# Optimization experiments

Measured on AMD Instinct MI355X. Metric: run time of the kernel, lower is better.

## Reference

```python
import jax, jax.numpy as jnp
import numpy as np

B, T, D = 2, 2048, 2048
H, G, HD = 16, 4, 128
SCALE = 0.08838834764831845  # 1/sqrt(head_dim)
THETA = 10000.0
EPS = 1e-10


def _rope(x):
    # x: [B, T, h, HD]; faithful to source: cos/sin built from cat([freqs, freqs])
    hd = x.shape[-1]
    pos = jnp.arange(x.shape[1], dtype=x.dtype)
    inv_freq = 1.0 / (THETA ** (jnp.arange(0, hd, 2, dtype=x.dtype) / hd))
    freqs = pos[:, None] * inv_freq[None, :]            # [T, hd/2]
    emb = jnp.concatenate([freqs, freqs], axis=-1)      # [T, hd]
    cos = jnp.cos(emb)[None, :, None, :]
    sin = jnp.sin(emb)[None, :, None, :]
    x_even, x_odd = x[..., ::2], x[..., 1::2]
    rotated = jnp.stack((-x_odd, x_even), axis=-1).reshape(x.shape)
    return x * cos + rotated * sin


def _qk_norm(x):
    # F.normalize(p=2): x / clamp_min(||x||, eps)
    n = jnp.sqrt(jnp.sum(x * x, axis=-1, keepdims=True))
    return x / jnp.maximum(n, EPS)


def setup_inputs() -> dict:
    key = jax.random.key(0)
    k1, k2, k3 = jax.random.split(key, 3)
    x = jax.random.normal(k1, (B, T, D), dtype=jnp.float32)
    w_qkv = jax.random.normal(k2, (H * HD + 2 * G * HD, D), dtype=jnp.float32) * 0.02
    w_o = jax.random.normal(k3, (D, D), dtype=jnp.float32) * 0.02
    padding_mask = jnp.ones((B, T), dtype=bool)
    return {"x": x, "w_qkv": w_qkv, "w_o": w_o, "padding_mask": padding_mask,
            "use_qk_norm": 1, "use_mqa": 0}


def reference(x, w_qkv, w_o, padding_mask, use_qk_norm, use_mqa):
    qkv = jnp.einsum('btd,ed->bte', x, w_qkv)           # fused QKV projection
    q = qkv[..., :H * HD].reshape(B, T, H, HD)
    k = qkv[..., H * HD:H * HD + G * HD].reshape(B, T, G, HD)
    v = qkv[..., H * HD + G * HD:].reshape(B, T, G, HD)
    if use_qk_norm:
        q = _qk_norm(q)
        k = _qk_norm(k)
    q = _rope(q)
    k = _rope(k)
    if not use_mqa:
        rep = H // G
        k = jnp.repeat(k, rep, axis=2)                  # [B, T, H, HD]
        v = jnp.repeat(v, rep, axis=2)
    # attention: scores [B, H, Tq, Tk]
    scores = jnp.einsum('bqhd,bkhd->bhqk', q, k) * SCALE
    # faithful mask expansion: padding_mask[:, None, :, None] -> [B,1,Tq,Tk]
    mask = padding_mask[:, None, :, None]
    scores = jnp.where(mask, scores, jnp.finfo(scores.dtype).min)
    attn = jax.nn.softmax(scores, axis=-1)
    out = jnp.einsum('bhqk,bkhd->bqhd', attn, v).reshape(B, T, D)
    return jnp.einsum('btd,od->bto', out, w_o)
```

## Files before the change

### kernel.cpp

```cpp
#include <hip/hip_runtime.h>
#include <hip/hip_bf16.h>
#include <math.h>

#define B_SZ 2
#define T_SEQ 2048
#define D_MODEL 2048
#define NH 16
#define NG 4
#define HD 128
#define E_QKV 3072
#define SCALE_F 0.08838834764831845f

typedef __attribute__((ext_vector_type(8))) short short8;
typedef __attribute__((ext_vector_type(8))) _Float16 half8;
typedef __attribute__((ext_vector_type(4))) float f32x4;
typedef __attribute__((ext_vector_type(16))) float f32x16;
typedef __attribute__((ext_vector_type(4))) uint uint4v;

__device__ inline ushort f2bf(float f) {
    union { float f; uint u; } v; v.f = f;
    uint r = (v.u + 0x7FFFu + ((v.u >> 16) & 1u)) >> 16;
    return (ushort)r;
}
__device__ inline ushort f2h(float f) {
    union { _Float16 h; ushort u; } v;
    v.h = (_Float16)f;
    return v.u;
}

__device__ inline void glds16(const void* g, void* l) {
    __builtin_amdgcn_global_load_lds(
        (const __attribute__((address_space(1))) unsigned int*)g,
        (__attribute__((address_space(3))) unsigned int*)l,
        16, 0, 0);
}

__device__ inline uint cvtpk(float a, float b) {
    uint r;
    asm("v_cvt_pk_bf16_f32 %0, %1, %2" : "=v"(r) : "v"(a), "v"(b));
    return r;
}
__device__ inline void pl32swap(uint& a, uint& b) {
    asm("v_permlane32_swap_b32 %0, %1" : "+v"(a), "+v"(b));
}

__global__ __launch_bounds__(256) void cvt_f16_all(const float* __restrict__ x,
                                                   const float* __restrict__ wq,
                                                   const float* __restrict__ wo,
                                                   ushort* __restrict__ x16,
                                                   ushort* __restrict__ wq16,
                                                   ushort* __restrict__ wo16,
                                                   int n4x, int n4q, int n4o) {
    int i = blockIdx.x * 256 + threadIdx.x;
    const float* src;
    ushort* dst;
    if (i < n4x)                { src = x;  dst = x16; }
    else if (i < n4x + n4q)     { src = wq; dst = wq16; i -= n4x; }
    else if (i < n4x + n4q + n4o) { src = wo; dst = wo16; i -= n4x + n4q; }
    else return;
    float4 v = ((const float4*)src)[i];
    uint2 ho;
    ho.x = (uint)f2h(v.x) | ((uint)f2h(v.y) << 16);
    ho.y = (uint)f2h(v.z) | ((uint)f2h(v.w) << 16);
    ((uint2*)dst)[i] = ho;
}

__global__ __launch_bounds__(256) void rope_tab(float2* __restrict__ Rt) {
    int i = blockIdx.x * 256 + threadIdx.x;
    if (i >= T_SEQ * 64) return;
    int t = i >> 6, j = i & 63;
    float inv_freq = exp2f(-0.2076205059304595f * (float)j);
    float sn, cs;
    sincosf((float)t * inv_freq, &sn, &cs);
    Rt[i] = make_float2(cs, sn);
}

template <bool QKV>
__global__ __launch_bounds__(256, 3)
void gemm_f16(const ushort* __restrict__ A,
              const ushort* __restrict__ B,
              float* __restrict__ C,
              ushort* __restrict__ Qb,
              ushort* __restrict__ Kb,
              ushort* __restrict__ Vt,
              const float2* __restrict__ Rt,
              int M, int N, int K) {
    __shared__ __attribute__((aligned(16))) ushort smem[16384];
    ushort* sA = smem;
    ushort* sB = smem + 8192;

    const int tid  = threadIdx.x;
    const int wave = tid >> 6;
    const int lane = tid & 63;
    const int c    = lane & 15;
    const int quad = lane >> 4;
    const int wr   = wave >> 1;
    const int wc   = wave & 1;
    const size_t m0 = (size_t)blockIdx.y * 128;
    const size_t n0 = (size_t)blockIdx.x * 128;

    const int srow = lane >> 3;
    const int sg   = ((lane & 7) ^ (srow & 7)) * 8;
    const ushort* gsrc;
    ushort* sdst;
    if (wave < 2) {
        gsrc = A + (m0 + wave * 64 + srow) * (size_t)K + sg;
        sdst = sA + wave * 4096;
    } else {
        gsrc = B + (n0 + (wave - 2) * 64 + srow) * (size_t)K + sg;
        sdst = sB + (wave - 2) * 4096;
    }

    f32x4 acc[4][4];
#pragma unroll
    for (int i = 0; i < 4; ++i)
#pragma unroll
        for (int j = 0; j < 4; ++j) acc[i][j] = (f32x4){0.f, 0.f, 0.f, 0.f};

    const int cg = c & 7;

    for (int k0 = 0; k0 < K; k0 += 64) {
        if (k0) __syncthreads();
#pragma unroll
        for (int i = 0; i < 8; ++i)
            glds16(gsrc + (size_t)(i * 8) * K + k0, sdst + i * 512);
        __syncthreads();

#pragma unroll
        for (int ks = 0; ks < 2; ++ks) {
            const int ga = ((ks * 4 + quad) ^ cg) * 8;
            half8 fa[4];
#pragma unroll
            for (int mi = 0; mi < 4; ++mi)
                fa[mi] = *(const half8*)&sA[(wr * 64 + mi * 16 + c) * 64 + ga];
#pragma unroll
            for (int ni = 0; ni < 4; ++ni) {
                half8 fb = *(const half8*)&sB[(wc * 64 + ni * 16 + c) * 64 + ga];
#pragma unroll
                for (int mi = 0; mi < 4; ++mi)
                    acc[mi][ni] = __builtin_amdgcn_mfma_f32_16x16x32_f16(fa[mi], fb, acc[mi][ni], 0, 0, 0);
            }
        }
    }

    if constexpr (!QKV) {
#pragma unroll
        for (int mi = 0; mi < 4; ++mi)
#pragma unroll
            for (int ni = 0; ni < 4; ++ni)
#pragma unroll
                for (int r = 0; r < 4; ++r)
                    C[(m0 + wr * 64 + mi * 16 + quad * 4 + r) * N + n0 + wc * 64 + ni * 16 + c] =
                        acc[mi][ni][r];
        return;
    } else {
        const int hq = blockIdx.x;
        const int gmBase = (int)m0 + wr * 64;
        __syncthreads();

        if (hq < NH + NG) {
            float ps[4][4];
#pragma unroll
            for (int mi = 0; mi < 4; ++mi)
#pragma unroll
                for (int r = 0; r < 4; ++r) {
                    float s = 0.f;
#pragma unroll
                    for (int ni = 0; ni < 4; ++ni) {
                        float v = acc[mi][ni][r];
                        s += v * v;
                    }
#pragma unroll
                    for (int o = 1; o < 16; o <<= 1) s += __shfl_xor(s, o);
                    ps[mi][r] = s;
                }
            float* red = (float*)smem;
            if (c == 0) {
#pragma unroll
                for (int mi = 0; mi < 4; ++mi)
#pragma unroll
                    for (int r = 0; r < 4; ++r)
                        red[wave * 64 + mi * 16 + quad * 4 + r] = ps[mi][r];
            }
            __syncthreads();

            const int hb = (hq < NH) ? hq : hq - NH;

#pragma unroll
            for (int mi = 0; mi < 4; ++mi)
#pragma unroll
                for (int r = 0; r < 4; ++r) {
                    const int rid = mi * 16 + quad * 4 + r;
                    float s2 = red[wave * 64 + rid] + red[(wave ^ 1) * 64 + rid];
                    float inv = 1.f / fmaxf(sqrtf(s2), 1e-10f);
                    const int gm = gmBase + rid;
                    const int b = gm >> 11, t = gm & (T_SEQ - 1);
                    const float2* rt = Rt + (size_t)t * 64;
#pragma unroll
                    for (int ni = 0; ni < 4; ++ni) {
                        float nx = acc[mi][ni][r] * inv;
                        float2 cs2 = rt[ni * 16 + c];
                        float nb = __shfl_xor(nx, 1);
                        float rot = (c & 1) ? nb : -nb;
                        float val = nx * cs2.x + rot * cs2.y;
                        const int d = wc * 64 + ni * 16 + c;
                        if (hq < NH)
                            Qb[(((size_t)b * NH + hb) * T_SEQ + t) * HD + d] = f2bf(val * SCALE_F);
                        else
                            Kb[(((size_t)b * NG + hb) * T_SEQ + t) * HD + d] = f2bf(val);
                    }
                }
        } else {
            const int g  = hq - (NH + NG);
            const int b  = (int)(m0 >> 11);
            const int t0 = (int)(m0 & (T_SEQ - 1));
            const int bg = b * NG + g;
            const int dd = wave * 32 + (lane >> 1);
            const int th = lane & 1;
#pragma unroll
            for (int pass = 0; pass < 2; ++pass) {
                if (wr == pass) {
#pragma unroll
                    for (int mi = 0; mi < 4; ++mi)
#pragma unroll
                        for (int ni = 0; ni < 4; ++ni) {
                            uint2 w;
                            w.x = cvtpk(acc[mi][ni][0], acc[mi][ni][1]);
                            w.y = cvtpk(acc[mi][ni][2], acc[mi][ni][3]);
                            const int d  = wc * 64 + ni * 16 + c;
                            const int tl = mi * 16 + quad * 4;
                            *(uint2*)&smem[d * 72 + tl] = w;
                        }
                }
                __syncthreads();
                size_t vb = ((size_t)bg * HD + dd) * T_SEQ + t0 + pass * 64 + th * 32;
#pragma unroll
                for (int k = 0; k < 4; ++k) {
                    short8 v = *(const short8*)&smem[dd * 72 + th * 32 + k * 8];
                    *(short8*)&Vt[vb + k * 8] = v;
                }
                __syncthreads();
            }
        }
    }
}

__global__ __launch_bounds__(256, 2) void attn_mfma4(const ushort* __restrict__ Qb,
                                                     const ushort* __restrict__ Kb,
                                                     const ushort* __restrict__ Vt,
                                                     ushort* __restrict__ AOh) {
    __shared__ __attribute__((aligned(16))) ushort Ks[2][64 * 128];
    __shared__ __attribute__((aligned(16))) ushort Vts[2][128 * 64 + 128];

    const int qt   = blockIdx.x;
    const int h    = blockIdx.y;
    const int b    = blockIdx.z;
    const int g    = h >> 2;
    const int tid  = threadIdx.x;
    const int wave = tid >> 6;
    const int lane = tid & 63;
    const int l31  = lane & 31;
    const int hi   = lane >> 5;
    const int wq   = wave * 32;

    const ushort* Qg = Qb + (((size_t)b * NH + h) * T_SEQ + qt * 128) * HD;
    const ushort* Kg = Kb + ((size_t)b * NG + g) * T_SEQ * HD;
    const ushort* Vg = Vt + ((size_t)b * NG + g) * (size_t)HD * T_SEQ;

    int goK[8];
#pragma unroll
    for (int s = 0; s < 8; ++s) goK[s] = ((2 * s + hi) ^ (l31 & 15)) * 8;
    int vbase[4];
#pragma unroll
    for (int db = 0; db < 4; ++db)
        vbase[db] = (db * 32 + l31) * 64 + (db * 4 + (l31 >> 3)) * 8;
    int goV[4];
#pragma unroll
    for (int s4 = 0; s4 < 4; ++s4) goV[s4] = ((2 * s4 + hi) ^ (l31 & 7)) * 8;

    auto stage = [&](int buf, int kt) {
#pragma unroll
        for (int i = 0; i < 4; ++i) {
            int row = wave * 16 + i * 4 + (lane >> 4);
            glds16(Kg + (size_t)(kt + row) * HD + (((lane & 15) ^ (row & 15)) * 8),
                   &Ks[buf][(wave * 16 + i * 4) * 128]);
        }
#pragma unroll
        for (int i = 0; i < 4; ++i) {
            int row = wave * 32 + i * 8 + (lane >> 3);
            int iss = wave * 4 + i;
            glds16(Vg + (size_t)row * T_SEQ + kt + (((lane & 7) ^ (row & 7)) * 8),
                   &Vts[buf][(size_t)iss * 520]);
        }
    };

    stage(0, 0);

    short8 qf[8];
#pragma unroll
    for (int s = 0; s < 8; ++s)
        qf[s] = *(const short8*)&Qg[(size_t)(wq + l31) * HD + s * 16 + hi * 8];

    f32x16 O[4];
#pragma unroll
    for (int i = 0; i < 4; ++i)
#pragma unroll
        for (int r = 0; r < 16; ++r) O[i][r] = 0.f;
    float lp = 0.f;

    __syncthreads();

    for (int t = 0; t < T_SEQ / 64; ++t) {
        const int cur = t & 1;
        if (t + 1 < T_SEQ / 64) stage(cur ^ 1, (t + 1) * 64);

        const ushort* KsC = Ks[cur];
        const ushort* VtC = Vts[cur];

        f32x16 S0, S1;
#pragma unroll
        for (int r = 0; r < 16; ++r) { S0[r] = 0.f; S1[r] = 0.f; }

        __builtin_amdgcn_s_setprio(1);
#pragma unroll
        for (int s = 0; s < 8; ++s) {
            short8 kf0 = *(const short8*)&KsC[l31 * 128 + goK[s]];
            short8 kf1 = *(const short8*)&KsC[(32 + l31) * 128 + goK[s]];
            S0 = __builtin_amdgcn_mfma_f32_32x32x16_bf16(kf0, qf[s], S0, 0, 0, 0);
            S1 = __builtin_amdgcn_mfma_f32_32x32x16_bf16(kf1, qf[s], S1, 0, 0, 0);
        }
        __builtin_amdgcn_s_setprio(0);

        short8 pa[4];
        {
            float p[16];
#pragma unroll
            for (int r = 0; r < 16; ++r) { p[r] = __expf(S0[r]); lp += p[r]; }
            uint c0 = cvtpk(p[0], p[1]),   c1 = cvtpk(p[2], p[3]);
            uint c2 = cvtpk(p[4], p[5]),   c3 = cvtpk(p[6], p[7]);
            uint c4 = cvtpk(p[8], p[9]),   c5 = cvtpk(p[10], p[11]);
            uint c6 = cvtpk(p[12], p[13]), c7 = cvtpk(p[14], p[15]);
            pl32swap(c0, c2); pl32swap(c1, c3);
            pl32swap(c4, c6); pl32swap(c5, c7);
            union { uint4v u; short8 s8; } ua, ub;
            ua.u = (uint4v){c0, c1, c2, c3};
            ub.u = (uint4v){c4, c5, c6, c7};
            pa[0] = ua.s8; pa[1] = ub.s8;
        }
        {
            float p[16];
#pragma unroll
            for (int r = 0; r < 16; ++r) { p[r] = __expf(S1[r]); lp += p[r]; }
            uint c0 = cvtpk(p[0], p[1]),   c1 = cvtpk(p[2], p[3]);
            uint c2 = cvtpk(p[4], p[5]),   c3 = cvtpk(p[6], p[7]);
            uint c4 = cvtpk(p[8], p[9]),   c5 = cvtpk(p[10], p[11]);
            uint c6 = cvtpk(p[12], p[13]), c7 = cvtpk(p[14], p[15]);
            pl32swap(c0, c2); pl32swap(c1, c3);
            pl32swap(c4, c6); pl32swap(c5, c7);
            union { uint4v u; short8 s8; } ua, ub;
            ua.u = (uint4v){c0, c1, c2, c3};
            ub.u = (uint4v){c4, c5, c6, c7};
            pa[2] = ua.s8; pa[3] = ub.s8;
        }

        __builtin_amdgcn_s_setprio(1);
#pragma unroll
        for (int db = 0; db < 4; ++db)
#pragma unroll
            for (int s4 = 0; s4 < 4; ++s4) {
                short8 vf = *(const short8*)&VtC[vbase[db] + goV[s4]];
                O[db] = __builtin_amdgcn_mfma_f32_32x32x16_bf16(pa[s4], vf, O[db], 0, 0, 0);
            }
        __builtin_amdgcn_s_setprio(0);

        __syncthreads();
    }

    lp += __shfl_xor(lp, 32);
    float inv = 1.f / lp;
#pragma unroll
    for (int r = 0; r < 16; ++r) {
        int qp = (r & 3) + 8 * (r >> 2) + 4 * hi;
        float iv = __shfl(inv, qp);
        size_t idx = ((size_t)b * T_SEQ + qt * 128 + wq + qp) * D_MODEL + h * HD + l31;
#pragma unroll
        for (int db = 0; db < 4; ++db)
            AOh[idx + db * 32] = f2h(O[db][r] * iv);
    }
}

extern "C" void kernel_launch(void* const* d_in, const int* in_sizes, int n_in,
                              void* d_out, int out_size, void* d_ws, size_t ws_size,
                              hipStream_t stream) {
    const float* x      = (const float*)d_in[0];
    const float* w_qkv  = (const float*)d_in[1];
    const float* w_o    = (const float*)d_in[2];

    float* out = (float*)d_out;

    const int M = B_SZ * T_SEQ;
    const size_t nX  = (size_t)M * D_MODEL;
    const size_t nWq = (size_t)E_QKV * D_MODEL;
    const size_t nWo = (size_t)D_MODEL * D_MODEL;

    ushort* x16  = (ushort*)d_ws;
    ushort* aoh  = x16 + nX;
    ushort* wq16 = aoh + nX;
    ushort* wo16 = wq16 + nWq;
    ushort* Qb   = wo16 + nWo;
    ushort* Kb   = Qb + (size_t)B_SZ * NH * T_SEQ * HD;
    ushort* Vt   = Kb + (size_t)B_SZ * NG * T_SEQ * HD;
    float2* Rt   = (float2*)(Vt + (size_t)B_SZ * NG * (size_t)HD * T_SEQ);

    rope_tab<<<(T_SEQ * 64 + 255) / 256, 256, 0, stream>>>(Rt);
    {
        int n4x = (int)(nX / 4), n4q = (int)(nWq / 4), n4o = (int)(nWo / 4);
        int nb = (n4x + n4q + n4o + 255) / 256;
        cvt_f16_all<<<nb, 256, 0, stream>>>(x, w_qkv, w_o, x16, wq16, wo16, n4x, n4q, n4o);
    }

    {
        dim3 grid(E_QKV / 128, M / 128);
        gemm_f16<true><<<grid, 256, 0, stream>>>(x16, wq16,
                                                 nullptr, Qb, Kb, Vt, Rt,
                                                 M, E_QKV, D_MODEL);
    }
    {
        dim3 grid(T_SEQ / 128, NH, B_SZ);
        attn_mfma4<<<grid, 256, 0, stream>>>(Qb, Kb, Vt, aoh);
    }
    {
        dim3 grid(D_MODEL / 128, M / 128);
        gemm_f16<false><<<grid, 256, 0, stream>>>(aoh, wo16,
                                                  out, nullptr, nullptr, nullptr, nullptr,
                                                  M, D_MODEL, D_MODEL);
    }
}
```

Before: 199.2 us.

## Double-buffer GEMM shared-memory tiles with K-step of 32

Converts the single-buffered GEMM main loop into a two-stage ping-pong pipeline. The next K-slice is loaded into the alternate LDS buffer while MFMAs run on the current one. The K-step shrinks from 64 to 32 so both buffers fit in the same LDS footprint, and the swizzle is adjusted to match. Global-load latency can now overlap compute, but the loop runs twice as many iterations, each with a barrier and fewer MFMAs to hide latency.

```diff
diff --git a/kernel.cpp b/kernel.cpp
--- a/kernel.cpp
+++ b/kernel.cpp
@@ -77,17 +77,15 @@
 
 template <bool QKV>
 __global__ __launch_bounds__(256, 3)
-void gemm_f16(const ushort* __restrict__ A,
-              const ushort* __restrict__ B,
-              float* __restrict__ C,
-              ushort* __restrict__ Qb,
-              ushort* __restrict__ Kb,
-              ushort* __restrict__ Vt,
-              const float2* __restrict__ Rt,
-              int M, int N, int K) {
-    __shared__ __attribute__((aligned(16))) ushort smem[16384];
-    ushort* sA = smem;
-    ushort* sB = smem + 8192;
+void gemm_f16_db(const ushort* __restrict__ A,
+                 const ushort* __restrict__ B,
+                 float* __restrict__ C,
+                 ushort* __restrict__ Qb,
+                 ushort* __restrict__ Kb,
+                 ushort* __restrict__ Vt,
+                 const float2* __restrict__ Rt,
+                 int M, int N, int K) {
+    __shared__ __attribute__((aligned(16))) ushort smem[2][8192];
 
     const int tid  = threadIdx.x;
     const int wave = tid >> 6;
@@ -99,17 +97,11 @@
     const size_t m0 = (size_t)blockIdx.y * 128;
     const size_t n0 = (size_t)blockIdx.x * 128;
 
-    const int srow = lane >> 3;
-    const int sg   = ((lane & 7) ^ (srow & 7)) * 8;
-    const ushort* gsrc;
-    ushort* sdst;
-    if (wave < 2) {
-        gsrc = A + (m0 + wave * 64 + srow) * (size_t)K + sg;
-        sdst = sA + wave * 4096;
-    } else {
-        gsrc = B + (n0 + (wave - 2) * 64 + srow) * (size_t)K + sg;
-        sdst = sB + (wave - 2) * 4096;
-    }
+    const int lrow = lane >> 2;
+    const int gch  = ((lane & 3) ^ ((lane >> 3) & 3)) * 8;
+    const ushort* gT   = (wave < 2) ? A + m0 * (size_t)K : B + n0 * (size_t)K;
+    const ushort* gsrc = gT + (size_t)((wave & 1) * 64 + lrow) * K + gch;
+    const int sbase = (wave >= 2 ? 4096 : 0) + (wave & 1) * 2048;
 
     f32x4 acc[4][4];
 #pragma unroll
@@ -117,30 +109,35 @@
 #pragma unroll
         for (int j = 0; j < 4; ++j) acc[i][j] = (f32x4){0.f, 0.f, 0.f, 0.f};
 
-    const int cg = c & 7;
-
-    for (int k0 = 0; k0 < K; k0 += 64) {
-        if (k0) __syncthreads();
-#pragma unroll
-        for (int i = 0; i < 8; ++i)
-            glds16(gsrc + (size_t)(i * 8) * K + k0, sdst + i * 512);
+    const int go = (quad ^ ((c >> 1) & 3)) * 8;
+
+#pragma unroll
+    for (int i = 0; i < 4; ++i)
+        glds16(gsrc + (size_t)(i * 16) * K, &smem[0][sbase + i * 512]);
+    __syncthreads();
+
+    int buf = 0;
+    for (int k0 = 0; k0 < K; k0 += 32) {
+        if (k0 + 32 < K) {
+#pragma unroll
+            for (int i = 0; i < 4; ++i)
+                glds16(gsrc + (size_t)(i * 16) * K + (k0 + 32), &smem[buf ^ 1][sbase + i * 512]);
+        }
+        const ushort* sA = smem[buf];
+        const ushort* sB = smem[buf] + 4096;
+        half8 fa[4];
+#pragma unroll
+        for (int mi = 0; mi < 4; ++mi)
+            fa[mi] = *(const half8*)&sA[(wr * 64 + mi * 16 + c) * 32 + go];
+#pragma unroll
+        for (int ni = 0; ni < 4; ++ni) {
+            half8 fb = *(const half8*)&sB[(wc * 64 + ni * 16 + c) * 32 + go];
+#pragma unroll
+            for (int mi = 0; mi < 4; ++mi)
+                acc[mi][ni] = __builtin_amdgcn_mfma_f32_16x16x32_f16(fa[mi], fb, acc[mi][ni], 0, 0, 0);
+        }
         __syncthreads();
-
-#pragma unroll
-        for (int ks = 0; ks < 2; ++ks) {
-            const int ga = ((ks * 4 + quad) ^ cg) * 8;
-            half8 fa[4];
-#pragma unroll
-            for (int mi = 0; mi < 4; ++mi)
-                fa[mi] = *(const half8*)&sA[(wr * 64 + mi * 16 + c) * 64 + ga];
-#pragma unroll
-            for (int ni = 0; ni < 4; ++ni) {
-                half8 fb = *(const half8*)&sB[(wc * 64 + ni * 16 + c) * 64 + ga];
-#pragma unroll
-                for (int mi = 0; mi < 4; ++mi)
-                    acc[mi][ni] = __builtin_amdgcn_mfma_f32_16x16x32_f16(fa[mi], fb, acc[mi][ni], 0, 0, 0);
-            }
-        }
+        buf ^= 1;
     }
 
     if constexpr (!QKV) {
@@ -154,9 +151,9 @@
                         acc[mi][ni][r];
         return;
     } else {
+        ushort* scratch = (ushort*)smem;
         const int hq = blockIdx.x;
         const int gmBase = (int)m0 + wr * 64;
-        __syncthreads();
 
         if (hq < NH + NG) {
             float ps[4][4];
@@ -174,7 +171,7 @@
                     for (int o = 1; o < 16; o <<= 1) s += __shfl_xor(s, o);
                     ps[mi][r] = s;
                 }
-            float* red = (float*)smem;
+            float* red = (float*)scratch;
             if (c == 0) {
 #pragma unroll
                 for (int mi = 0; mi < 4; ++mi)
@@ -229,14 +226,14 @@
                             w.y = cvtpk(acc[mi][ni][2], acc[mi][ni][3]);
                             const int d  = wc * 64 + ni * 16 + c;
                             const int tl = mi * 16 + quad * 4;
-                            *(uint2*)&smem[d * 72 + tl] = w;
+                            *(uint2*)&scratch[d * 72 + tl] = w;
                         }
                 }
                 __syncthreads();
                 size_t vb = ((size_t)bg * HD + dd) * T_SEQ + t0 + pass * 64 + th * 32;
 #pragma unroll
                 for (int k = 0; k < 4; ++k) {
-                    short8 v = *(const short8*)&smem[dd * 72 + th * 32 + k * 8];
+                    short8 v = *(const short8*)&scratch[dd * 72 + th * 32 + k * 8];
                     *(short8*)&Vt[vb + k * 8] = v;
                 }
                 __syncthreads();
@@ -421,9 +418,9 @@
 
     {
         dim3 grid(E_QKV / 128, M / 128);
-        gemm_f16<true><<<grid, 256, 0, stream>>>(x16, wq16,
-                                                 nullptr, Qb, Kb, Vt, Rt,
-                                                 M, E_QKV, D_MODEL);
+        gemm_f16_db<true><<<grid, 256, 0, stream>>>(x16, wq16,
+                                                    nullptr, Qb, Kb, Vt, Rt,
+                                                    M, E_QKV, D_MODEL);
     }
     {
         dim3 grid(T_SEQ / 128, NH, B_SZ);
@@ -431,8 +428,8 @@
     }
     {
         dim3 grid(D_MODEL / 128, M / 128);
-        gemm_f16<false><<<grid, 256, 0, stream>>>(aoh, wo16,
-                                                  out, nullptr, nullptr, nullptr, nullptr,
-                                                  M, D_MODEL, D_MODEL);
-    }
-}
+        gemm_f16_db<false><<<grid, 256, 0, stream>>>(aoh, wo16,
+                                                     out, nullptr, nullptr, nullptr, nullptr,
+                                                     M, D_MODEL, D_MODEL);
+    }
+}
```

After: 211.2 us. +6.0%, slower.
